# Kernel tuning notes

Measured on AMD Instinct MI355X. Metric: run time of the kernel, lower is better.

The kernel has to match this reference:

```python
import jax, jax.numpy as jnp
import numpy as np
from jax import lax

# Dims fixed by the module: Linear(96,24) => 16 channels * (24/4) length => per-step feature L=24
L = 24

def _conv1d(x, w, b):
    # x: (N, Cin, L), w: (Cout, Cin, K), 'same' padding for K=3
    y = lax.conv_general_dilated(x, w, window_strides=(1,), padding=[(1, 1)],
                                 dimension_numbers=("NCH", "OIH", "NCH"))
    return y + b[None, :, None]

def _maxpool2(x):
    # x: (N, C, L) -> (N, C, L//2), non-overlapping window of 2
    n, c, l = x.shape
    return x.reshape(n, c, l // 2, 2).max(axis=-1)

def setup_inputs() -> dict:
    key = jax.random.key(0)
    ks = jax.random.split(key, 11)
    S, B = 512, 256
    def u(k, shape, fan_in):
        bound = 1.0 / np.sqrt(fan_in)
        return jax.random.uniform(k, shape, jnp.float32, -bound, bound)
    return {
        "x":   jax.random.normal(ks[0], (S, B, L), jnp.float32),
        "w11": u(ks[1], (8, 1, 3), 1 * 3),   "b11": u(ks[2], (8,), 1 * 3),
        "w12": u(ks[3], (8, 8, 3), 8 * 3),   "b12": u(ks[4], (8,), 8 * 3),
        "w21": u(ks[5], (16, 8, 3), 8 * 3),  "b21": u(ks[6], (16,), 8 * 3),
        "w22": u(ks[7], (16, 16, 3), 16 * 3), "b22": u(ks[8], (16,), 16 * 3),
        "Wl":  u(ks[9], (24, 96), 96),        "bl": u(ks[10], (24,), 96),
    }

def reference(x, w11, b11, w12, b12, w21, b21, w22, b22, Wl, bl):
    # Original loops over timesteps applying the same CNN; timestep and batch
    # are independent, so fuse them into one conv batch (identical math).
    S, B, Lf = x.shape
    h = x.reshape(S * B, 1, Lf)                 # (SB, 1, 24)
    h = jax.nn.relu(_conv1d(h, w11, b11))       # (SB, 8, 24); Dropout(0.1) = identity in eval
    h = jax.nn.relu(_conv1d(h, w12, b12))       # (SB, 8, 24)
    h = _maxpool2(h)                            # (SB, 8, 12)
    h = jax.nn.relu(_conv1d(h, w21, b21))       # (SB, 16, 12); Dropout = identity in eval
    h = jax.nn.relu(_conv1d(h, w22, b22))       # (SB, 16, 12)
    h = _maxpool2(h)                            # (SB, 16, 6)
    h = h.reshape(S, B, 96)                     # torch reshape(batch, -1) per step
    return h @ Wl.T + bl                        # (S, B, 24)
```

## Files before the change

kernel.cpp:

```cpp
#include <hip/hip_runtime.h>


#define TPB 256

__launch_bounds__(TPB, 2)
__global__ void cnn_pre_lstm_kernel(
    const float* __restrict__ x,
    const float* __restrict__ w11, const float* __restrict__ b11,
    const float* __restrict__ w12, const float* __restrict__ b12,
    const float* __restrict__ w21, const float* __restrict__ b21,
    const float* __restrict__ w22, const float* __restrict__ b22,
    const float* __restrict__ Wl,  const float* __restrict__ bl,
    float* __restrict__ out)
{
    __shared__ float sA[12288];
    __shared__ float sB[6144];

    const int tid = threadIdx.x;
    const int ln  = tid & 63;
    const int wv  = __builtin_amdgcn_readfirstlane(tid >> 6);

    {
        const float* xg = x + (size_t)blockIdx.x * (64 * 24);
        #pragma unroll
        for (int k = 0; k < 6; ++k) {
            int o = tid + k * TPB;
            int s = o / 24, p = o % 24;
            sB[s * 25 + p] = xg[o];
        }
    }
    __syncthreads();

    {
        const int co0 = wv * 2;
        float wA0 = w11[co0*3+0], wA1 = w11[co0*3+1], wA2 = w11[co0*3+2];
        float wB0 = w11[(co0+1)*3+0], wB1 = w11[(co0+1)*3+1], wB2 = w11[(co0+1)*3+2];
        float bA = b11[co0], bB = b11[co0+1];

        float xm = 0.f, xc = sB[ln*25 + 0], xp;
        #pragma unroll
        for (int p = 0; p < 24; ++p) {
            xp = (p < 23) ? sB[ln*25 + p + 1] : 0.f;
            float a = fmaf(wA0, xm, fmaf(wA1, xc, fmaf(wA2, xp, bA)));
            float b = fmaf(wB0, xm, fmaf(wB1, xc, fmaf(wB2, xp, bB)));
            sA[ co0      * 1536 + p * 64 + ln] = fmaxf(a, 0.f);
            sA[(co0 + 1) * 1536 + p * 64 + ln] = fmaxf(b, 0.f);
            xm = xc; xc = xp;
        }
    }
    __syncthreads();

    {
        const int co0 = wv * 2;
        float acc[2][24];
        #pragma unroll
        for (int i = 0; i < 2; ++i) {
            float bb = b12[co0 + i];
            #pragma unroll
            for (int p = 0; p < 24; ++p) acc[i][p] = bb;
        }
        for (int ci = 0; ci < 8; ++ci) {
            float wg[2][3];
            #pragma unroll
            for (int i = 0; i < 2; ++i) {
                const float* wp = w12 + ((co0 + i) * 8 + ci) * 3;
                wg[i][0] = wp[0]; wg[i][1] = wp[1]; wg[i][2] = wp[2];
            }
            const int cb = ci * 1536 + ln;
            float xm = 0.f, xc = sA[cb], xp;
            #pragma unroll
            for (int p = 0; p < 24; ++p) {
                xp = (p < 23) ? sA[cb + (p + 1) * 64] : 0.f;
                #pragma unroll
                for (int i = 0; i < 2; ++i)
                    acc[i][p] = fmaf(wg[i][0], xm, fmaf(wg[i][1], xc, fmaf(wg[i][2], xp, acc[i][p])));
                xm = xc; xc = xp;
            }
        }
        #pragma unroll
        for (int i = 0; i < 2; ++i)
            #pragma unroll
            for (int p2 = 0; p2 < 12; ++p2)
                sB[(co0 + i) * 768 + p2 * 64 + ln] =
                    fmaxf(fmaxf(acc[i][2*p2], acc[i][2*p2+1]), 0.f);
    }
    __syncthreads();

    {
        const int co0 = wv * 4;
        float acc[4][12];
        #pragma unroll
        for (int i = 0; i < 4; ++i) {
            float bb = b21[co0 + i];
            #pragma unroll
            for (int p = 0; p < 12; ++p) acc[i][p] = bb;
        }
        for (int ci = 0; ci < 8; ++ci) {
            float wg[4][3];
            #pragma unroll
            for (int i = 0; i < 4; ++i) {
                const float* wp = w21 + ((co0 + i) * 8 + ci) * 3;
                wg[i][0] = wp[0]; wg[i][1] = wp[1]; wg[i][2] = wp[2];
            }
            const int cb = ci * 768 + ln;
            float xm = 0.f, xc = sB[cb], xp;
            #pragma unroll
            for (int p = 0; p < 12; ++p) {
                xp = (p < 11) ? sB[cb + (p + 1) * 64] : 0.f;
                #pragma unroll
                for (int i = 0; i < 4; ++i)
                    acc[i][p] = fmaf(wg[i][0], xm, fmaf(wg[i][1], xc, fmaf(wg[i][2], xp, acc[i][p])));
                xm = xc; xc = xp;
            }
        }
        #pragma unroll
        for (int i = 0; i < 4; ++i)
            #pragma unroll
            for (int p = 0; p < 12; ++p)
                sA[(co0 + i) * 768 + p * 64 + ln] = fmaxf(acc[i][p], 0.f);
    }
    __syncthreads();

    {
        const int co0 = wv * 4;
        float acc[4][12];
        #pragma unroll
        for (int i = 0; i < 4; ++i) {
            float bb = b22[co0 + i];
            #pragma unroll
            for (int p = 0; p < 12; ++p) acc[i][p] = bb;
        }
        for (int ci = 0; ci < 16; ++ci) {
            float wg[4][3];
            #pragma unroll
            for (int i = 0; i < 4; ++i) {
                const float* wp = w22 + ((co0 + i) * 16 + ci) * 3;
                wg[i][0] = wp[0]; wg[i][1] = wp[1]; wg[i][2] = wp[2];
            }
            const int cb = ci * 768 + ln;
            float xm = 0.f, xc = sA[cb], xp;
            #pragma unroll
            for (int p = 0; p < 12; ++p) {
                xp = (p < 11) ? sA[cb + (p + 1) * 64] : 0.f;
                #pragma unroll
                for (int i = 0; i < 4; ++i)
                    acc[i][p] = fmaf(wg[i][0], xm, fmaf(wg[i][1], xc, fmaf(wg[i][2], xp, acc[i][p])));
                xm = xc; xc = xp;
            }
        }
        #pragma unroll
        for (int i = 0; i < 4; ++i)
            #pragma unroll
            for (int p2 = 0; p2 < 6; ++p2)
                sB[(co0 + i) * 384 + p2 * 64 + ln] =
                    fmaxf(fmaxf(acc[i][2*p2], acc[i][2*p2+1]), 0.f);
    }
    __syncthreads();

    {
        const int j0 = wv * 6;
        float acc6[6];
        #pragma unroll
        for (int i = 0; i < 6; ++i) acc6[i] = bl[j0 + i];
        for (int c = 0; c < 16; ++c) {
            #pragma unroll
            for (int p = 0; p < 6; ++p) {
                float v = sB[c * 384 + p * 64 + ln];
                const int f = c * 6 + p;
                #pragma unroll
                for (int i = 0; i < 6; ++i)
                    acc6[i] = fmaf(Wl[(j0 + i) * 96 + f], v, acc6[i]);
            }
        }
        #pragma unroll
        for (int i = 0; i < 6; ++i)
            sA[ln * 24 + j0 + i] = acc6[i];
    }
    __syncthreads();

    {
        float* og = out + (size_t)blockIdx.x * (64 * 24);
        #pragma unroll
        for (int k = 0; k < 6; ++k) {
            int o = tid + k * TPB;
            og[o] = sA[o];
        }
    }
}

extern "C" void kernel_launch(void* const* d_in, const int* in_sizes, int n_in,
                              void* d_out, int out_size, void* d_ws, size_t ws_size,
                              hipStream_t stream) {
    const float* x   = (const float*)d_in[0];
    const float* w11 = (const float*)d_in[1];
    const float* b11 = (const float*)d_in[2];
    const float* w12 = (const float*)d_in[3];
    const float* b12 = (const float*)d_in[4];
    const float* w21 = (const float*)d_in[5];
    const float* b21 = (const float*)d_in[6];
    const float* w22 = (const float*)d_in[7];
    const float* b22 = (const float*)d_in[8];
    const float* Wl  = (const float*)d_in[9];
    const float* bl  = (const float*)d_in[10];
    float* out = (float*)d_out;

    const int n_samples = in_sizes[0] / 24;
    const int blocks = n_samples / 64;

    hipLaunchKernelGGL(cnn_pre_lstm_kernel, dim3(blocks), dim3(TPB), 0, stream,
                       x, w11, b11, w12, b12, w21, b21, w22, b22, Wl, bl, out);
}
```

Baseline: 163.6 us.

## Store conv activations as packed fp16 pairs and use fdot2 accumulation

Intermediate activations are packed two channels per 32-bit word in fp16, which halves shared memory. The three inner conv layers use v_dot2 (fp16 pair dot with fp32 accumulate), roughly halving FMA count and LDS reads. Launch bounds are raised to allow three blocks per CU, and the linear layer now reads weights as float4 with a padded output staging buffer. Rounding activations and weights to fp16 adds precision error against the fp32 reference.

```diff
diff --git a/kernel.cpp b/kernel.cpp
--- a/kernel.cpp
+++ b/kernel.cpp
@@ -1,9 +1,22 @@
 #include <hip/hip_runtime.h>
 
 
+typedef _Float16 h2v __attribute__((ext_vector_type(2)));
+
+__device__ __forceinline__ float fdot2(h2v a, h2v b, float c) {
+    return __builtin_amdgcn_fdot2(a, b, c, false);
+}
+__device__ __forceinline__ unsigned packh2(float a, float b) {
+    h2v p; p.x = (_Float16)a; p.y = (_Float16)b;
+    return __builtin_bit_cast(unsigned, p);
+}
+__device__ __forceinline__ h2v ldh2(unsigned u) {
+    return __builtin_bit_cast(h2v, u);
+}
+
 #define TPB 256
 
-__launch_bounds__(TPB, 2)
+__launch_bounds__(TPB, 3)
 __global__ void cnn_pre_lstm_kernel(
     const float* __restrict__ x,
     const float* __restrict__ w11, const float* __restrict__ b11,
@@ -13,177 +26,219 @@
     const float* __restrict__ Wl,  const float* __restrict__ bl,
     float* __restrict__ out)
 {
-    __shared__ float sA[12288];
-    __shared__ float sB[6144];
+    __shared__ unsigned sA_[6144];
+    __shared__ unsigned sB_[3072];
+    float* sInF  = (float*)sB_;
+    float* sOutF = (float*)sA_;
 
     const int tid = threadIdx.x;
     const int ln  = tid & 63;
     const int wv  = __builtin_amdgcn_readfirstlane(tid >> 6);
 
     {
-        const float* xg = x + (size_t)blockIdx.x * (64 * 24);
+        const float* xg = x + (size_t)blockIdx.x * 1536;
         #pragma unroll
         for (int k = 0; k < 6; ++k) {
             int o = tid + k * TPB;
             int s = o / 24, p = o % 24;
-            sB[s * 25 + p] = xg[o];
-        }
-    }
-    __syncthreads();
-
-    {
-        const int co0 = wv * 2;
-        float wA0 = w11[co0*3+0], wA1 = w11[co0*3+1], wA2 = w11[co0*3+2];
-        float wB0 = w11[(co0+1)*3+0], wB1 = w11[(co0+1)*3+1], wB2 = w11[(co0+1)*3+2];
-        float bA = b11[co0], bB = b11[co0+1];
-
-        float xm = 0.f, xc = sB[ln*25 + 0], xp;
+            sInF[s * 25 + p] = xg[o];
+        }
+    }
+    __syncthreads();
+
+    {
+        const int c0 = 2 * wv;
+        const float wA0 = w11[c0*3+0], wA1 = w11[c0*3+1], wA2 = w11[c0*3+2];
+        const float wB0 = w11[c0*3+3], wB1 = w11[c0*3+4], wB2 = w11[c0*3+5];
+        const float bA = b11[c0], bB = b11[c0+1];
+
+        float xv[24];
+        #pragma unroll
+        for (int p = 0; p < 24; ++p) xv[p] = sInF[ln*25 + p];
+
         #pragma unroll
         for (int p = 0; p < 24; ++p) {
-            xp = (p < 23) ? sB[ln*25 + p + 1] : 0.f;
-            float a = fmaf(wA0, xm, fmaf(wA1, xc, fmaf(wA2, xp, bA)));
-            float b = fmaf(wB0, xm, fmaf(wB1, xc, fmaf(wB2, xp, bB)));
-            sA[ co0      * 1536 + p * 64 + ln] = fmaxf(a, 0.f);
-            sA[(co0 + 1) * 1536 + p * 64 + ln] = fmaxf(b, 0.f);
-            xm = xc; xc = xp;
-        }
-    }
-    __syncthreads();
-
-    {
-        const int co0 = wv * 2;
+            float a = bA, b = bB;
+            if (p > 0)  { a = fmaf(wA0, xv[p-1], a); b = fmaf(wB0, xv[p-1], b); }
+            a = fmaf(wA1, xv[p], a);  b = fmaf(wB1, xv[p], b);
+            if (p < 23) { a = fmaf(wA2, xv[p+1], a); b = fmaf(wB2, xv[p+1], b); }
+            sA_[wv*1536 + p*64 + ln] = packh2(fmaxf(a, 0.f), fmaxf(b, 0.f));
+        }
+    }
+    __syncthreads();
+
+    {
+        const int c0 = 2 * wv;
+        h2v wp[2][4][3];
+        #pragma unroll
+        for (int i = 0; i < 2; ++i)
+            #pragma unroll
+            for (int cp = 0; cp < 4; ++cp)
+                #pragma unroll
+                for (int k = 0; k < 3; ++k) {
+                    const float* wr = w12 + (c0 + i) * 24;
+                    wp[i][cp][k] = ldh2(packh2(wr[(2*cp)*3 + k], wr[(2*cp+1)*3 + k]));
+                }
         float acc[2][24];
-        #pragma unroll
-        for (int i = 0; i < 2; ++i) {
-            float bb = b12[co0 + i];
-            #pragma unroll
-            for (int p = 0; p < 24; ++p) acc[i][p] = bb;
-        }
-        for (int ci = 0; ci < 8; ++ci) {
-            float wg[2][3];
-            #pragma unroll
-            for (int i = 0; i < 2; ++i) {
-                const float* wp = w12 + ((co0 + i) * 8 + ci) * 3;
-                wg[i][0] = wp[0]; wg[i][1] = wp[1]; wg[i][2] = wp[2];
-            }
-            const int cb = ci * 1536 + ln;
-            float xm = 0.f, xc = sA[cb], xp;
+        {
+            const float bb0 = b12[c0], bb1 = b12[c0+1];
+            #pragma unroll
+            for (int p = 0; p < 24; ++p) { acc[0][p] = bb0; acc[1][p] = bb1; }
+        }
+        #pragma unroll
+        for (int cp = 0; cp < 4; ++cp) {
+            h2v xv[24];
+            #pragma unroll
+            for (int p = 0; p < 24; ++p) xv[p] = ldh2(sA_[cp*1536 + p*64 + ln]);
             #pragma unroll
             for (int p = 0; p < 24; ++p) {
-                xp = (p < 23) ? sA[cb + (p + 1) * 64] : 0.f;
-                #pragma unroll
-                for (int i = 0; i < 2; ++i)
-                    acc[i][p] = fmaf(wg[i][0], xm, fmaf(wg[i][1], xc, fmaf(wg[i][2], xp, acc[i][p])));
-                xm = xc; xc = xp;
-            }
-        }
-        #pragma unroll
-        for (int i = 0; i < 2; ++i)
-            #pragma unroll
-            for (int p2 = 0; p2 < 12; ++p2)
-                sB[(co0 + i) * 768 + p2 * 64 + ln] =
-                    fmaxf(fmaxf(acc[i][2*p2], acc[i][2*p2+1]), 0.f);
-    }
-    __syncthreads();
-
-    {
-        const int co0 = wv * 4;
+                #pragma unroll
+                for (int i = 0; i < 2; ++i) {
+                    if (p > 0)  acc[i][p] = fdot2(wp[i][cp][0], xv[p-1], acc[i][p]);
+                    acc[i][p] = fdot2(wp[i][cp][1], xv[p], acc[i][p]);
+                    if (p < 23) acc[i][p] = fdot2(wp[i][cp][2], xv[p+1], acc[i][p]);
+                }
+            }
+        }
+        #pragma unroll
+        for (int q = 0; q < 12; ++q) {
+            float r0 = fmaxf(fmaxf(acc[0][2*q], acc[0][2*q+1]), 0.f);
+            float r1 = fmaxf(fmaxf(acc[1][2*q], acc[1][2*q+1]), 0.f);
+            sB_[wv*768 + q*64 + ln] = packh2(r0, r1);
+        }
+    }
+    __syncthreads();
+
+    {
+        const int c0 = 4 * wv;
+        h2v wp[4][4][3];
+        #pragma unroll
+        for (int i = 0; i < 4; ++i)
+            #pragma unroll
+            for (int cp = 0; cp < 4; ++cp)
+                #pragma unroll
+                for (int k = 0; k < 3; ++k) {
+                    const float* wr = w21 + (c0 + i) * 24;
+                    wp[i][cp][k] = ldh2(packh2(wr[(2*cp)*3 + k], wr[(2*cp+1)*3 + k]));
+                }
         float acc[4][12];
         #pragma unroll
         for (int i = 0; i < 4; ++i) {
-            float bb = b21[co0 + i];
+            const float bb = b21[c0 + i];
             #pragma unroll
             for (int p = 0; p < 12; ++p) acc[i][p] = bb;
         }
-        for (int ci = 0; ci < 8; ++ci) {
-            float wg[4][3];
-            #pragma unroll
-            for (int i = 0; i < 4; ++i) {
-                const float* wp = w21 + ((co0 + i) * 8 + ci) * 3;
-                wg[i][0] = wp[0]; wg[i][1] = wp[1]; wg[i][2] = wp[2];
-            }
-            const int cb = ci * 768 + ln;
-            float xm = 0.f, xc = sB[cb], xp;
+        #pragma unroll
+        for (int cp = 0; cp < 4; ++cp) {
+            h2v xv[12];
+            #pragma unroll
+            for (int p = 0; p < 12; ++p) xv[p] = ldh2(sB_[cp*768 + p*64 + ln]);
             #pragma unroll
             for (int p = 0; p < 12; ++p) {
-                xp = (p < 11) ? sB[cb + (p + 1) * 64] : 0.f;
-                #pragma unroll
-                for (int i = 0; i < 4; ++i)
-                    acc[i][p] = fmaf(wg[i][0], xm, fmaf(wg[i][1], xc, fmaf(wg[i][2], xp, acc[i][p])));
-                xm = xc; xc = xp;
-            }
-        }
-        #pragma unroll
-        for (int i = 0; i < 4; ++i)
+                #pragma unroll
+                for (int i = 0; i < 4; ++i) {
+                    if (p > 0)  acc[i][p] = fdot2(wp[i][cp][0], xv[p-1], acc[i][p]);
+                    acc[i][p] = fdot2(wp[i][cp][1], xv[p], acc[i][p]);
+                    if (p < 11) acc[i][p] = fdot2(wp[i][cp][2], xv[p+1], acc[i][p]);
+                }
+            }
+        }
+        #pragma unroll
+        for (int pr = 0; pr < 2; ++pr)
             #pragma unroll
             for (int p = 0; p < 12; ++p)
-                sA[(co0 + i) * 768 + p * 64 + ln] = fmaxf(acc[i][p], 0.f);
-    }
-    __syncthreads();
-
-    {
-        const int co0 = wv * 4;
+                sA_[(2*wv + pr)*768 + p*64 + ln] =
+                    packh2(fmaxf(acc[2*pr][p], 0.f), fmaxf(acc[2*pr+1][p], 0.f));
+    }
+    __syncthreads();
+
+    {
+        const int c0 = 4 * wv;
         float acc[4][12];
         #pragma unroll
         for (int i = 0; i < 4; ++i) {
-            float bb = b22[co0 + i];
+            const float bb = b22[c0 + i];
             #pragma unroll
             for (int p = 0; p < 12; ++p) acc[i][p] = bb;
         }
-        for (int ci = 0; ci < 16; ++ci) {
-            float wg[4][3];
-            #pragma unroll
-            for (int i = 0; i < 4; ++i) {
-                const float* wp = w22 + ((co0 + i) * 16 + ci) * 3;
-                wg[i][0] = wp[0]; wg[i][1] = wp[1]; wg[i][2] = wp[2];
-            }
-            const int cb = ci * 768 + ln;
-            float xm = 0.f, xc = sA[cb], xp;
-            #pragma unroll
-            for (int p = 0; p < 12; ++p) {
-                xp = (p < 11) ? sA[cb + (p + 1) * 64] : 0.f;
-                #pragma unroll
-                for (int i = 0; i < 4; ++i)
-                    acc[i][p] = fmaf(wg[i][0], xm, fmaf(wg[i][1], xc, fmaf(wg[i][2], xp, acc[i][p])));
-                xm = xc; xc = xp;
-            }
-        }
-        #pragma unroll
-        for (int i = 0; i < 4; ++i)
-            #pragma unroll
-            for (int p2 = 0; p2 < 6; ++p2)
-                sB[(co0 + i) * 384 + p2 * 64 + ln] =
-                    fmaxf(fmaxf(acc[i][2*p2], acc[i][2*p2+1]), 0.f);
-    }
-    __syncthreads();
-
-    {
-        const int j0 = wv * 6;
+        #pragma unroll
+        for (int hh = 0; hh < 2; ++hh) {
+            h2v wp[4][4][3];
+            #pragma unroll
+            for (int i = 0; i < 4; ++i)
+                #pragma unroll
+                for (int cp = 0; cp < 4; ++cp)
+                    #pragma unroll
+                    for (int k = 0; k < 3; ++k) {
+                        const float* wr = w22 + (c0 + i) * 48;
+                        const int ci0 = 2 * (4*hh + cp);
+                        wp[i][cp][k] = ldh2(packh2(wr[ci0*3 + k], wr[(ci0+1)*3 + k]));
+                    }
+            #pragma unroll
+            for (int cp = 0; cp < 4; ++cp) {
+                const int gcp = 4*hh + cp;
+                h2v xv[12];
+                #pragma unroll
+                for (int p = 0; p < 12; ++p) xv[p] = ldh2(sA_[gcp*768 + p*64 + ln]);
+                #pragma unroll
+                for (int p = 0; p < 12; ++p) {
+                    #pragma unroll
+                    for (int i = 0; i < 4; ++i) {
+                        if (p > 0)  acc[i][p] = fdot2(wp[i][cp][0], xv[p-1], acc[i][p]);
+                        acc[i][p] = fdot2(wp[i][cp][1], xv[p], acc[i][p]);
+                        if (p < 11) acc[i][p] = fdot2(wp[i][cp][2], xv[p+1], acc[i][p]);
+                    }
+                }
+            }
+        }
+        #pragma unroll
+        for (int pr = 0; pr < 2; ++pr)
+            #pragma unroll
+            for (int q = 0; q < 6; ++q) {
+                float r0 = fmaxf(fmaxf(acc[2*pr][2*q],   acc[2*pr][2*q+1]),   0.f);
+                float r1 = fmaxf(fmaxf(acc[2*pr+1][2*q], acc[2*pr+1][2*q+1]), 0.f);
+                sB_[(2*wv + pr)*384 + q*64 + ln] = packh2(r0, r1);
+            }
+    }
+    __syncthreads();
+
+    {
+        const int j0 = 6 * wv;
+        float v[96];
+        #pragma unroll
+        for (int cp = 0; cp < 8; ++cp)
+            #pragma unroll
+            for (int q = 0; q < 6; ++q) {
+                h2v t = ldh2(sB_[cp*384 + q*64 + ln]);
+                v[12*cp + q]     = (float)t.x;
+                v[12*cp + q + 6] = (float)t.y;
+            }
         float acc6[6];
         #pragma unroll
         for (int i = 0; i < 6; ++i) acc6[i] = bl[j0 + i];
-        for (int c = 0; c < 16; ++c) {
-            #pragma unroll
-            for (int p = 0; p < 6; ++p) {
-                float v = sB[c * 384 + p * 64 + ln];
-                const int f = c * 6 + p;
-                #pragma unroll
-                for (int i = 0; i < 6; ++i)
-                    acc6[i] = fmaf(Wl[(j0 + i) * 96 + f], v, acc6[i]);
+        #pragma unroll
+        for (int i = 0; i < 6; ++i) {
+            const float4* wr = (const float4*)(Wl + (j0 + i) * 96);
+            #pragma unroll
+            for (int g = 0; g < 24; ++g) {
+                float4 w4 = wr[g];
+                acc6[i] = fmaf(w4.x, v[4*g+0], fmaf(w4.y, v[4*g+1],
+                          fmaf(w4.z, v[4*g+2], fmaf(w4.w, v[4*g+3], acc6[i]))));
             }
         }
         #pragma unroll
         for (int i = 0; i < 6; ++i)
-            sA[ln * 24 + j0 + i] = acc6[i];
-    }
-    __syncthreads();
-
-    {
-        float* og = out + (size_t)blockIdx.x * (64 * 24);
+            sOutF[ln*25 + j0 + i] = acc6[i];
+    }
+    __syncthreads();
+
+    {
+        float* og = out + (size_t)blockIdx.x * 1536;
         #pragma unroll
         for (int k = 0; k < 6; ++k) {
             int o = tid + k * TPB;
-            og[o] = sA[o];
+            int s = o / 24, j = o % 24;
+            og[o] = sOutF[s*25 + j];
         }
     }
 }
```

Measured after the change: 138.8 us. 1.18x faster.
